# Kernel tuning notes

Hardware: AMD Instinct MI355X
Metric: run time of the kernel (lower is better)

## Reference

```python
import jax, jax.numpy as jnp
import numpy as np
from jax import lax

B, T, N, D = 64, 128, 64, 64
Q, EMB, PLM = 5, 8, 768
ALPHA = 0.5  # rarity_alpha

def _mlp(x, W1, b1, W2, b2):
    return jax.nn.relu(x @ W1 + b1) @ W2 + b2

def setup_inputs() -> dict:
    key = jax.random.key(0)
    ks = jax.random.split(key, 16)
    def xav(k, shape):
        fan_in = shape[-2] if len(shape) > 1 else shape[0]
        return jax.random.normal(k, shape, jnp.float32) / np.sqrt(fan_in)
    obs_emb = jax.random.normal(ks[0], (B, T, N, D), jnp.float32)
    observed_mask = (jax.random.uniform(ks[1], (B, T, N)) < 0.5).astype(jnp.float32)
    lengths = jax.random.randint(ks[2], (B, 1), T // 2, T + 1).astype(jnp.int32)
    lengths = lengths.at[0, 0].set(T)  # ensure max(lengths) == T like torch loop bound
    avg_interval = jax.random.uniform(ks[3], (B, T, N), jnp.float32) * 10.0
    return {
        "obs_emb": obs_emb, "observed_mask": observed_mask,
        "lengths": lengths, "avg_interval": avg_interval,
        "var_plm_rep": jax.random.normal(ks[4], (N, PLM), jnp.float32),
        "rarity_W": jax.random.normal(ks[5], (N, N), jnp.float32),
        "Wf1": xav(ks[6], (PLM, 2 * D)), "bf1": jnp.zeros((2 * D,), jnp.float32),
        "Wf2": xav(ks[7], (2 * D, Q)), "bf2": jnp.zeros((Q,), jnp.float32),
        "Wg1": xav(ks[8], (PLM, 2 * D)), "bg1": jnp.zeros((2 * D,), jnp.float32),
        "Wg2": xav(ks[9], (2 * D, EMB)), "bg2": jnp.zeros((EMB,), jnp.float32),
        "Wu": xav(ks[10], (Q, 2 * D + 1, D)), "bu": xav(ks[11], (Q, D)),
        "Wr": xav(ks[12], (Q, 2 * D + 1, D)), "br": xav(ks[13], (Q, D)),
        "Wc": xav(ks[14], (Q, 2 * D + 1, D)), "bc": xav(ks[15], (Q, D)),
    }

def reference(obs_emb, observed_mask, lengths, avg_interval, var_plm_rep, rarity_W,
              Wf1, bf1, Wf2, bf2, Wg1, bg1, Wg2, bg2, Wu, bu, Wr, br, Wc, bc):
    Bb, Tt, Nn, Dd = obs_emb.shape
    m_all = observed_mask.astype(obs_emb.dtype)                 # [B,T,N]
    # plm reps are repeated across batch in torch -> batch-identical, keep [N,*]
    qv = _mlp(var_plm_rep, Wf1, bf1, Wf2, bf2)                  # [N,Q]
    ne = _mlp(var_plm_rep, Wg1, bg1, Wg2, bg2)                  # [N,EMB]
    ne = ne / jnp.linalg.norm(ne, axis=-1, keepdims=True)
    adj = jax.nn.softmax(ne @ ne.T, axis=-1)                    # [N,N]
    # time-invariant per-node hypernetwork weights (MLP_Param einsums hoisted)
    Wr_n = jnp.einsum('nq,qio->nio', qv, Wr); br_n = qv @ br    # [N,2D+1,D],[N,D]
    Wu_n = jnp.einsum('nq,qio->nio', qv, Wu); bu_n = qv @ bu
    Wc_n = jnp.einsum('nq,qio->nio', qv, Wc); bc_n = qv @ bc
    I = jnp.eye(Nn, dtype=obs_emb.dtype)
    var_total = m_all.sum(axis=1)                               # [B,N]
    lens = lengths[:, 0]

    def step(carry, inp):
        h, out = carry
        x_t, m_t, ai_t, t = inp                                 # [B,N,D],[B,N],[B,N],[]
        rs = ALPHA * jnp.tanh(ai_t / (var_total + 1.0))         # rarity score [B,N]
        x = jnp.concatenate([x_t, rs[..., None]], axis=-1)      # [B,N,D+1]
        combined = jnp.concatenate([x, h], axis=-1)             # [B,N,2D+1]
        R = -rarity_W[None] * jnp.abs(rs[:, :, None] - rs[:, None, :])
        am = m_t[:, :, None] * m_t[:, None, :]                  # masked adjacency support
        A = adj[None] * (1.0 + R) * am * (1.0 - I) + I          # [B,N,N]
        msg = jnp.einsum('bij,bjf->bif', A, combined)           # dense message passing
        r = jax.nn.sigmoid(jnp.einsum('bnf,nfo->bno', msg, Wr_n) + br_n)
        u = jax.nn.sigmoid(jnp.einsum('bnf,nfo->bno', msg, Wu_n) + bu_n)
        upd = m_t[..., None] > 0                                # observed-node scatter mask
        h_r = jnp.where(upd, r * h, h)
        comb2 = jnp.concatenate([x, h_r], axis=-1)              # NOTE: no adj matmul here (as in torch)
        cand = jnp.tanh(jnp.einsum('bnf,nfo->bno', comb2, Wc_n) + bc_n)
        h_new = jnp.where(upd, (1.0 - u) * h_r + u * cand, h)
        out_new = jnp.where((t == lens - 1)[:, None, None], h_new, out)
        return (h_new, out_new), None

    h0 = jnp.zeros((Bb, Nn, Dd), obs_emb.dtype)
    xs = (obs_emb.swapaxes(0, 1), m_all.swapaxes(0, 1),
          avg_interval.swapaxes(0, 1), jnp.arange(Tt))
    (_, out), _ = lax.scan(step, (h0, jnp.zeros_like(h0)), xs)
    return out
```

## Files before the change

### kernel.cpp

```cpp
#include <hip/hip_runtime.h>
#include <cstddef>
#include <cstdint>

#define B_ 64
#define T_ 128
#define N_ 64
#define D_ 64
#define Q_ 5
#define E_ 8
#define P_ 768
#define H_ 128

typedef _Float16 f16;
typedef _Float16 f16x2 __attribute__((ext_vector_type(2)));
typedef _Float16 f16x4 __attribute__((ext_vector_type(4)));
typedef _Float16 f16x8 __attribute__((ext_vector_type(8)));
typedef float f32x4 __attribute__((ext_vector_type(4)));

__global__ void k_mlps(const float* __restrict__ vpr,
                       const float* __restrict__ Wf1, const float* __restrict__ bf1,
                       const float* __restrict__ Wf2, const float* __restrict__ bf2,
                       const float* __restrict__ Wg1, const float* __restrict__ bg1,
                       const float* __restrict__ Wg2, const float* __restrict__ bg2,
                       float* __restrict__ qv, float* __restrict__ neb) {
  int n = blockIdx.x;
  int tid = threadIdx.x;
  __shared__ float v[P_];
  __shared__ float hid[H_];
  __shared__ float tmp[E_];

  for (int i = tid; i < P_; i += 256) v[i] = vpr[n * P_ + i];
  __syncthreads();

  for (int j = tid; j < H_; j += 256) {
    float a = bf1[j];
#pragma unroll 8
    for (int i = 0; i < P_; ++i) a += v[i] * Wf1[i * H_ + j];
    hid[j] = fmaxf(a, 0.f);
  }
  __syncthreads();
  if (tid < Q_) {
    float a = bf2[tid];
    for (int j = 0; j < H_; ++j) a += hid[j] * Wf2[j * Q_ + tid];
    qv[n * Q_ + tid] = a;
  }
  __syncthreads();

  for (int j = tid; j < H_; j += 256) {
    float a = bg1[j];
#pragma unroll 8
    for (int i = 0; i < P_; ++i) a += v[i] * Wg1[i * H_ + j];
    hid[j] = fmaxf(a, 0.f);
  }
  __syncthreads();
  if (tid < E_) {
    float a = bg2[tid];
    for (int j = 0; j < H_; ++j) a += hid[j] * Wg2[j * E_ + tid];
    tmp[tid] = a;
  }
  __syncthreads();
  if (tid == 0) {
    float s = 0.f;
    for (int e = 0; e < E_; ++e) s += tmp[e] * tmp[e];
    float r = 1.f / sqrtf(s);
    for (int e = 0; e < E_; ++e) neb[n * E_ + e] = tmp[e] * r;
  }
}

__global__ void k_meta(const float* __restrict__ neb, const float* __restrict__ qv,
                       const float* __restrict__ br, const float* __restrict__ bu,
                       const float* __restrict__ bc,
                       const float* __restrict__ Wr, const float* __restrict__ Wu,
                       const float* __restrict__ Wc,
                       float* __restrict__ adj, float* __restrict__ brn,
                       float* __restrict__ bun, float* __restrict__ bcn,
                       float* __restrict__ WrsR, float* __restrict__ WrsU,
                       float* __restrict__ WrsC) {
  int n = blockIdx.x;
  int j = threadIdx.x;
  float s = 0.f;
#pragma unroll
  for (int e = 0; e < E_; ++e) s += neb[n * E_ + e] * neb[j * E_ + e];
  float m = s;
  for (int off = 32; off; off >>= 1) m = fmaxf(m, __shfl_xor(m, off));
  float ex = expf(s - m);
  float sum = ex;
  for (int off = 32; off; off >>= 1) sum += __shfl_xor(sum, off);
  adj[n * N_ + j] = ex / sum;

  float pr = 0.f, pu = 0.f, pc = 0.f;
  float wr = 0.f, wu = 0.f, wc = 0.f;
#pragma unroll
  for (int q = 0; q < Q_; ++q) {
    float qq = qv[n * Q_ + q];
    pr += qq * br[q * D_ + j];
    pu += qq * bu[q * D_ + j];
    pc += qq * bc[q * D_ + j];
    wr += qq * Wr[((size_t)q * 129 + 64) * D_ + j];
    wu += qq * Wu[((size_t)q * 129 + 64) * D_ + j];
    wc += qq * Wc[((size_t)q * 129 + 64) * D_ + j];
  }
  brn[n * D_ + j] = pr;
  bun[n * D_ + j] = pu;
  bcn[n * D_ + j] = pc;
  WrsR[n * D_ + j] = wr;
  WrsU[n * D_ + j] = wu;
  WrsC[n * D_ + j] = wc;
}

__global__ void k_pack(const float* __restrict__ Wr, const float* __restrict__ Wu,
                       const float* __restrict__ Wc, f16* __restrict__ Wpk) {
  int bid = blockIdx.x;
  int nt = bid & 3;
  int kt = (bid >> 2) & 3;
  int q = (bid >> 4) % 5;
  int g = bid / 80;
  const float* W = (g == 0) ? Wr : ((g == 1) ? Wu : Wc);
  int l = threadIdx.x;
  int co = 16 * nt + (l & 15);
  f16* dst = Wpk + (size_t)bid * 512 + l * 8;
#pragma unroll
  for (int e = 0; e < 8; ++e) {
    int k = 32 * kt + 8 * (l >> 4) + e;
    int f = k + (k >= 64);
    dst[e] = (f16)W[((size_t)q * 129 + f) * D_ + co];
  }
}

__global__ void k_vt(const float* __restrict__ mask, float* __restrict__ vt) {
  int b = blockIdx.x;
  int n = threadIdx.x;
  float s = 0.f;
  for (int t = 0; t < T_; ++t) s += mask[(b * T_ + t) * N_ + n];
  vt[b * N_ + n] = s;
}

__launch_bounds__(1024, 1)
__global__ void k_seq(const float* __restrict__ obs, const float* __restrict__ mask,
                      const int* __restrict__ lengths, const float* __restrict__ ai,
                      const float* __restrict__ adjG, const float* __restrict__ rarw,
                      const float* __restrict__ brn, const float* __restrict__ bun,
                      const float* __restrict__ bcn, const float* __restrict__ WrsR,
                      const float* __restrict__ WrsU, const float* __restrict__ WrsC,
                      const float* __restrict__ qv, const float* __restrict__ vt,
                      const f16* __restrict__ Wpk, float* __restrict__ out) {
  __shared__ __align__(16) f16 combT[128 * 72];
  __shared__ __align__(16) f16 AmatPre2[64 * 72];
  __shared__ __align__(16) f16 actA[64 * 136];
  __shared__ __align__(16) f16 xA[64 * 72];
  __shared__ __align__(16) f16 pre1[64 * 68];
  __shared__ __align__(16) f16 qvS[64 * 8];
  __shared__ float rsS[64];
  __shared__ float mS[64];
  __shared__ float vtS[64];
  __shared__ float mrS[64];

  const int tid = threadIdx.x;
  const int b = blockIdx.x;
  const int lane = tid & 63;
  const int wv = tid >> 6;
  const int lm = lane & 15;
  const int lq = lane >> 4;

  const int en = tid >> 4;
  const int eo = (tid & 15) * 4;

  float h[4] = {0.f, 0.f, 0.f, 0.f};

  f16x2 bRp[2], bUp[2], bCp[2], wRp[2], wUp[2], wCp[2];
  {
    float4 v;
    v = *(const float4*)(brn + en * D_ + eo);
    bRp[0] = f16x2{(f16)v.x, (f16)v.y}; bRp[1] = f16x2{(f16)v.z, (f16)v.w};
    v = *(const float4*)(bun + en * D_ + eo);
    bUp[0] = f16x2{(f16)v.x, (f16)v.y}; bUp[1] = f16x2{(f16)v.z, (f16)v.w};
    v = *(const float4*)(bcn + en * D_ + eo);
    bCp[0] = f16x2{(f16)v.x, (f16)v.y}; bCp[1] = f16x2{(f16)v.z, (f16)v.w};
    v = *(const float4*)(WrsR + en * D_ + eo);
    wRp[0] = f16x2{(f16)v.x, (f16)v.y}; wRp[1] = f16x2{(f16)v.z, (f16)v.w};
    v = *(const float4*)(WrsU + en * D_ + eo);
    wUp[0] = f16x2{(f16)v.x, (f16)v.y}; wUp[1] = f16x2{(f16)v.z, (f16)v.w};
    v = *(const float4*)(WrsC + en * D_ + eo);
    wCp[0] = f16x2{(f16)v.x, (f16)v.y}; wCp[1] = f16x2{(f16)v.z, (f16)v.w};
  }

  if (tid < 512) {
    int n = tid >> 3, q = tid & 7;
    qvS[n * 8 + q] = (q < Q_) ? (f16)qv[n * Q_ + q] : (f16)0.f;
  }
  if (tid < 64) vtS[tid] = vt[b * N_ + tid];
  for (int i = tid; i < 64 * 72; i += 1024) combT[64 * 72 + i] = (f16)0.f;
  const int lenm1 = lengths[b] - 1;
  __syncthreads();

  for (int t = 0; t < T_; ++t) {
    if (tid < 64) {
      float mv = mask[(b * T_ + t) * N_ + tid];
      float av = ai[(b * T_ + t) * N_ + tid];
      mS[tid] = mv;
      rsS[tid] = 0.5f * tanhf(av / (vtS[tid] + 1.f));
    }
    {
      float4 xv = *(const float4*)(obs + (size_t)(b * T_ + t) * (N_ * D_) + en * D_ + eo);
      f16x4 xh = {(f16)xv.x, (f16)xv.y, (f16)xv.z, (f16)xv.w};
      *(f16x4*)(xA + en * 72 + eo) = xh;
      combT[(eo + 0) * 72 + en] = xh[0];
      combT[(eo + 1) * 72 + en] = xh[1];
      combT[(eo + 2) * 72 + en] = xh[2];
      combT[(eo + 3) * 72 + en] = xh[3];
    }
    __syncthreads();

    {
      const int i = en, j0 = eo;
      float4 ad = *(const float4*)(adjG + i * N_ + j0);
      float4 rw = *(const float4*)(rarw + i * N_ + j0);
      float ri = rsS[i], mi = mS[i];
      float a0 = ad.x * (1.f - rw.x * fabsf(ri - rsS[j0 + 0])) * mi * mS[j0 + 0];
      float a1 = ad.y * (1.f - rw.y * fabsf(ri - rsS[j0 + 1])) * mi * mS[j0 + 1];
      float a2 = ad.z * (1.f - rw.z * fabsf(ri - rsS[j0 + 2])) * mi * mS[j0 + 2];
      float a3 = ad.w * (1.f - rw.w * fabsf(ri - rsS[j0 + 3])) * mi * mS[j0 + 3];
      if (i == j0 + 0) a0 = 1.f;
      if (i == j0 + 1) a1 = 1.f;
      if (i == j0 + 2) a2 = 1.f;
      if (i == j0 + 3) a3 = 1.f;
      f16x4 av = {(f16)a0, (f16)a1, (f16)a2, (f16)a3};
      *(f16x4*)(AmatPre2 + i * 72 + j0) = av;
    }
    __syncthreads();

    {
#pragma unroll
      for (int s = 0; s < 2; ++s) {
        int tt = wv * 2 + s;
        int mt = tt >> 3, ft = tt & 7;
        f32x4 acc = {0.f, 0.f, 0.f, 0.f};
#pragma unroll
        for (int kt = 0; kt < 2; ++kt) {
          int j0 = 8 * lq + 32 * kt;
          f16x8 aF = *(const f16x8*)(AmatPre2 + (lm + 16 * mt) * 72 + j0);
          f16x8 bF = *(const f16x8*)(combT + (lm + 16 * ft) * 72 + j0);
          acc = __builtin_amdgcn_mfma_f32_16x16x32_f16(aF, bF, acc, 0, 0, 0);
        }
        int row = 16 * mt + 4 * lq;
        int col = 16 * ft + lm;
        actA[(row + 0) * 136 + col] = (f16)acc[0];
        actA[(row + 1) * 136 + col] = (f16)acc[1];
        actA[(row + 2) * 136 + col] = (f16)acc[2];
        actA[(row + 3) * 136 + col] = (f16)acc[3];
      }
      if (wv == 15) {
        float s = 0.f;
        for (int j = 0; j < 64; j += 2) {
          f16x2 a2 = *(const f16x2*)(AmatPre2 + lane * 72 + j);
          s += (float)a2[0] * rsS[j] + (float)a2[1] * rsS[j + 1];
        }
        mrS[lane] = s;
      }
    }
    __syncthreads();

    f32x4 cacc[4];
    if (wv < 8) {
      const int g = wv >> 2;
      const int nt = wv & 3;
      f32x4 acc[4] = {{0.f, 0.f, 0.f, 0.f}, {0.f, 0.f, 0.f, 0.f},
                      {0.f, 0.f, 0.f, 0.f}, {0.f, 0.f, 0.f, 0.f}};
      f16x8 qh[4];
#pragma unroll
      for (int mt = 0; mt < 4; ++mt)
        qh[mt] = *(const f16x8*)(qvS + (lm + 16 * mt) * 8);
#pragma unroll
      for (int kt = 0; kt < 4; ++kt) {
        f16x8 aF[4];
#pragma unroll
        for (int mt = 0; mt < 4; ++mt)
          aF[mt] = *(const f16x8*)(actA + (lm + 16 * mt) * 136 + 8 * lq + 32 * kt);
#pragma unroll
        for (int q = 0; q < 5; ++q) {
          f16x8 wF = *(const f16x8*)(Wpk +
              ((size_t)(((g * 5 + q) * 4 + kt) * 4 + nt) * 64 + lane) * 8);
#pragma unroll
          for (int mt = 0; mt < 4; ++mt) {
            f16x8 as = aF[mt] * qh[mt][q];
            acc[mt] = __builtin_amdgcn_mfma_f32_16x16x32_f16(as, wF, acc[mt], 0, 0, 0);
          }
        }
      }
      f16* dst = g ? AmatPre2 : pre1;
#pragma unroll
      for (int mt = 0; mt < 4; ++mt) {
        int row = 16 * mt + 4 * lq;
        int col = 16 * nt + lm;
        dst[(row + 0) * 68 + col] = (f16)acc[mt][0];
        dst[(row + 1) * 68 + col] = (f16)acc[mt][1];
        dst[(row + 2) * 68 + col] = (f16)acc[mt][2];
        dst[(row + 3) * 68 + col] = (f16)acc[mt][3];
      }
    } else if (wv < 12) {
      const int nt = wv - 8;
#pragma unroll
      for (int mt = 0; mt < 4; ++mt) cacc[mt] = f32x4{0.f, 0.f, 0.f, 0.f};
      f16x8 qh[4];
#pragma unroll
      for (int mt = 0; mt < 4; ++mt)
        qh[mt] = *(const f16x8*)(qvS + (lm + 16 * mt) * 8);
#pragma unroll
      for (int kt = 0; kt < 2; ++kt) {
        f16x8 aF[4];
#pragma unroll
        for (int mt = 0; mt < 4; ++mt)
          aF[mt] = *(const f16x8*)(xA + (lm + 16 * mt) * 72 + 8 * lq + 32 * kt);
#pragma unroll
        for (int q = 0; q < 5; ++q) {
          f16x8 wF = *(const f16x8*)(Wpk +
              ((size_t)(((2 * 5 + q) * 4 + kt) * 4 + nt) * 64 + lane) * 8);
#pragma unroll
          for (int mt = 0; mt < 4; ++mt) {
            f16x8 as = aF[mt] * qh[mt][q];
            cacc[mt] = __builtin_amdgcn_mfma_f32_16x16x32_f16(as, wF, cacc[mt], 0, 0, 0);
          }
        }
      }
    }
    __syncthreads();

    float uq[4], hrq[4];
    const bool upd = mS[en] > 0.f;
    {
      f16x4 pR = *(const f16x4*)(pre1 + en * 68 + eo);
      f16x4 pU = *(const f16x4*)(AmatPre2 + en * 68 + eo);
      float mr = mrS[en];
      f16x4 hrh;
#pragma unroll
      for (int k = 0; k < 4; ++k) {
        float preR = (float)pR[k] + mr * (float)wRp[k >> 1][k & 1] + (float)bRp[k >> 1][k & 1];
        float preU = (float)pU[k] + mr * (float)wUp[k >> 1][k & 1] + (float)bUp[k >> 1][k & 1];
        float r = 1.f / (1.f + expf(-preR));
        float u = 1.f / (1.f + expf(-preU));
        float hr = upd ? r * h[k] : h[k];
        uq[k] = u;
        hrq[k] = hr;
        hrh[k] = (f16)hr;
      }
      *(f16x4*)(actA + en * 136 + 64 + eo) = hrh;
    }
    __syncthreads();

    if (wv >= 8 && wv < 12) {
      const int nt = wv - 8;
      f16x8 qh[4];
#pragma unroll
      for (int mt = 0; mt < 4; ++mt)
        qh[mt] = *(const f16x8*)(qvS + (lm + 16 * mt) * 8);
#pragma unroll
      for (int kt = 2; kt < 4; ++kt) {
        f16x8 aF[4];
#pragma unroll
        for (int mt = 0; mt < 4; ++mt)
          aF[mt] = *(const f16x8*)(actA + (lm + 16 * mt) * 136 + 8 * lq + 32 * kt);
#pragma unroll
        for (int q = 0; q < 5; ++q) {
          f16x8 wF = *(const f16x8*)(Wpk +
              ((size_t)(((2 * 5 + q) * 4 + kt) * 4 + nt) * 64 + lane) * 8);
#pragma unroll
          for (int mt = 0; mt < 4; ++mt) {
            f16x8 as = aF[mt] * qh[mt][q];
            cacc[mt] = __builtin_amdgcn_mfma_f32_16x16x32_f16(as, wF, cacc[mt], 0, 0, 0);
          }
        }
      }
#pragma unroll
      for (int mt = 0; mt < 4; ++mt) {
        int row = 16 * mt + 4 * lq;
        int col = 16 * nt + lm;
        pre1[(row + 0) * 68 + col] = (f16)cacc[mt][0];
        pre1[(row + 1) * 68 + col] = (f16)cacc[mt][1];
        pre1[(row + 2) * 68 + col] = (f16)cacc[mt][2];
        pre1[(row + 3) * 68 + col] = (f16)cacc[mt][3];
      }
    }
    __syncthreads();

    {
      f16x4 pC = *(const f16x4*)(pre1 + en * 68 + eo);
      float rsv = rsS[en];
#pragma unroll
      for (int k = 0; k < 4; ++k) {
        float pc = (float)pC[k] + rsv * (float)wCp[k >> 1][k & 1] + (float)bCp[k >> 1][k & 1];
        float cand = tanhf(pc);
        float hn = upd ? (1.f - uq[k]) * hrq[k] + uq[k] * cand : h[k];
        h[k] = hn;
        combT[(64 + eo + k) * 72 + en] = (f16)hn;
      }
      if (t == lenm1) {
        float4 o4 = {h[0], h[1], h[2], h[3]};
        *(float4*)(out + ((size_t)b * N_ + en) * D_ + eo) = o4;
      }
    }
    __syncthreads();
  }
}

extern "C" void kernel_launch(void* const* d_in, const int* in_sizes, int n_in,
                              void* d_out, int out_size, void* d_ws, size_t ws_size,
                              hipStream_t stream) {
  const float* obs  = (const float*)d_in[0];
  const float* mask = (const float*)d_in[1];
  const int*   lens = (const int*)d_in[2];
  const float* ai   = (const float*)d_in[3];
  const float* vpr  = (const float*)d_in[4];
  const float* rarw = (const float*)d_in[5];
  const float* Wf1 = (const float*)d_in[6],  *bf1 = (const float*)d_in[7];
  const float* Wf2 = (const float*)d_in[8],  *bf2 = (const float*)d_in[9];
  const float* Wg1 = (const float*)d_in[10], *bg1 = (const float*)d_in[11];
  const float* Wg2 = (const float*)d_in[12], *bg2 = (const float*)d_in[13];
  const float* Wu = (const float*)d_in[14], *bu = (const float*)d_in[15];
  const float* Wr = (const float*)d_in[16], *br = (const float*)d_in[17];
  const float* Wc = (const float*)d_in[18], *bc = (const float*)d_in[19];

  char* p = (char*)d_ws;
  auto carve = [&](size_t bytes) {
    char* r = p;
    p += (bytes + 255) & ~(size_t)255;
    return r;
  };
  float* qv   = (float*)carve(N_ * Q_ * 4);
  float* neb  = (float*)carve(N_ * E_ * 4);
  float* adj  = (float*)carve(N_ * N_ * 4);
  float* brn  = (float*)carve(N_ * D_ * 4);
  float* bun  = (float*)carve(N_ * D_ * 4);
  float* bcn  = (float*)carve(N_ * D_ * 4);
  float* WrsR = (float*)carve(N_ * D_ * 4);
  float* WrsU = (float*)carve(N_ * D_ * 4);
  float* WrsC = (float*)carve(N_ * D_ * 4);
  float* vt   = (float*)carve(B_ * N_ * 4);
  f16* Wpk    = (f16*)carve((size_t)3 * 5 * 4 * 4 * 64 * 8 * 2);

  k_mlps<<<N_, 256, 0, stream>>>(vpr, Wf1, bf1, Wf2, bf2, Wg1, bg1, Wg2, bg2, qv, neb);
  k_meta<<<N_, 64, 0, stream>>>(neb, qv, br, bu, bc, Wr, Wu, Wc,
                                adj, brn, bun, bcn, WrsR, WrsU, WrsC);
  k_pack<<<240, 64, 0, stream>>>(Wr, Wu, Wc, Wpk);
  k_vt<<<B_, 64, 0, stream>>>(mask, vt);
  k_seq<<<B_, 1024, 0, stream>>>(obs, mask, lens, ai, adj, rarw,
                                 brn, bun, bcn, WrsR, WrsU, WrsC,
                                 qv, vt, Wpk, (float*)d_out);
}
```

Measured before the change: 2.153 ms.

## Restructure recurrent kernel to 512 threads with register-resident weights and prefetch

```diff
diff --git a/kernel.cpp b/kernel.cpp
--- a/kernel.cpp
+++ b/kernel.cpp
@@ -16,6 +16,13 @@
 typedef _Float16 f16x4 __attribute__((ext_vector_type(4)));
 typedef _Float16 f16x8 __attribute__((ext_vector_type(8)));
 typedef float f32x4 __attribute__((ext_vector_type(4)));
+
+__device__ __forceinline__ float fast_sig(float x) {
+  return 1.f / (1.f + __expf(-x));
+}
+__device__ __forceinline__ float fast_tanh(float x) {
+  return 1.f - 2.f / (1.f + __expf(2.f * x));
+}
 
 __global__ void k_mlps(const float* __restrict__ vpr,
                        const float* __restrict__ Wf1, const float* __restrict__ bf1,
@@ -26,37 +33,36 @@
   int n = blockIdx.x;
   int tid = threadIdx.x;
   __shared__ float v[P_];
-  __shared__ float hid[H_];
+  __shared__ float hf[H_];
+  __shared__ float hg[H_];
   __shared__ float tmp[E_];
 
   for (int i = tid; i < P_; i += 256) v[i] = vpr[n * P_ + i];
   __syncthreads();
 
-  for (int j = tid; j < H_; j += 256) {
+  if (tid < H_) {
+    int j = tid;
     float a = bf1[j];
 #pragma unroll 8
     for (int i = 0; i < P_; ++i) a += v[i] * Wf1[i * H_ + j];
-    hid[j] = fmaxf(a, 0.f);
+    hf[j] = fmaxf(a, 0.f);
+  } else {
+    int j = tid - H_;
+    float a = bg1[j];
+#pragma unroll 8
+    for (int i = 0; i < P_; ++i) a += v[i] * Wg1[i * H_ + j];
+    hg[j] = fmaxf(a, 0.f);
   }
   __syncthreads();
   if (tid < Q_) {
     float a = bf2[tid];
-    for (int j = 0; j < H_; ++j) a += hid[j] * Wf2[j * Q_ + tid];
+    for (int j = 0; j < H_; ++j) a += hf[j] * Wf2[j * Q_ + tid];
     qv[n * Q_ + tid] = a;
-  }
-  __syncthreads();
-
-  for (int j = tid; j < H_; j += 256) {
-    float a = bg1[j];
-#pragma unroll 8
-    for (int i = 0; i < P_; ++i) a += v[i] * Wg1[i * H_ + j];
-    hid[j] = fmaxf(a, 0.f);
-  }
-  __syncthreads();
-  if (tid < E_) {
-    float a = bg2[tid];
-    for (int j = 0; j < H_; ++j) a += hid[j] * Wg2[j * E_ + tid];
-    tmp[tid] = a;
+  } else if (tid >= 8 && tid < 8 + E_) {
+    int e = tid - 8;
+    float a = bg2[e];
+    for (int j = 0; j < H_; ++j) a += hg[j] * Wg2[j * E_ + e];
+    tmp[e] = a;
   }
   __syncthreads();
   if (tid == 0) {
@@ -71,8 +77,8 @@
                        const float* __restrict__ br, const float* __restrict__ bu,
                        const float* __restrict__ bc,
                        const float* __restrict__ Wr, const float* __restrict__ Wu,
-                       const float* __restrict__ Wc,
-                       float* __restrict__ adj, float* __restrict__ brn,
+                       const float* __restrict__ Wc, const float* __restrict__ rarw,
+                       f16x2* __restrict__ adjP, float* __restrict__ brn,
                        float* __restrict__ bun, float* __restrict__ bcn,
                        float* __restrict__ WrsR, float* __restrict__ WrsU,
                        float* __restrict__ WrsC) {
@@ -83,10 +89,11 @@
   for (int e = 0; e < E_; ++e) s += neb[n * E_ + e] * neb[j * E_ + e];
   float m = s;
   for (int off = 32; off; off >>= 1) m = fmaxf(m, __shfl_xor(m, off));
-  float ex = expf(s - m);
+  float ex = __expf(s - m);
   float sum = ex;
   for (int off = 32; off; off >>= 1) sum += __shfl_xor(sum, off);
-  adj[n * N_ + j] = ex / sum;
+  float av = ex / sum;
+  adjP[n * N_ + j] = f16x2{(f16)av, (f16)(av * rarw[n * N_ + j])};
 
   float pr = 0.f, pu = 0.f, pc = 0.f;
   float wr = 0.f, wu = 0.f, wc = 0.f;
@@ -135,25 +142,24 @@
   vt[b * N_ + n] = s;
 }
 
-__launch_bounds__(1024, 1)
+__launch_bounds__(512, 1)
 __global__ void k_seq(const float* __restrict__ obs, const float* __restrict__ mask,
                       const int* __restrict__ lengths, const float* __restrict__ ai,
-                      const float* __restrict__ adjG, const float* __restrict__ rarw,
+                      const f16x2* __restrict__ adjP,
                       const float* __restrict__ brn, const float* __restrict__ bun,
                       const float* __restrict__ bcn, const float* __restrict__ WrsR,
                       const float* __restrict__ WrsU, const float* __restrict__ WrsC,
                       const float* __restrict__ qv, const float* __restrict__ vt,
                       const f16* __restrict__ Wpk, float* __restrict__ out) {
   __shared__ __align__(16) f16 combT[128 * 72];
-  __shared__ __align__(16) f16 AmatPre2[64 * 72];
   __shared__ __align__(16) f16 actA[64 * 136];
   __shared__ __align__(16) f16 xA[64 * 72];
-  __shared__ __align__(16) f16 pre1[64 * 68];
+  __shared__ __align__(16) f16 AP[64 * 72];
+  __shared__ __align__(16) f16 pCH[64 * 68];
   __shared__ __align__(16) f16 qvS[64 * 8];
-  __shared__ float rsS[64];
-  __shared__ float mS[64];
-  __shared__ float vtS[64];
-  __shared__ float mrS[64];
+  __shared__ float rsS[N_];
+  __shared__ float mS[N_];
+  __shared__ float mrS[N_];
 
   const int tid = threadIdx.x;
   const int b = blockIdx.x;
@@ -161,85 +167,134 @@
   const int wv = tid >> 6;
   const int lm = lane & 15;
   const int lq = lane >> 4;
-
-  const int en = tid >> 4;
-  const int eo = (tid & 15) * 4;
-
-  float h[4] = {0.f, 0.f, 0.f, 0.f};
-
-  f16x2 bRp[2], bUp[2], bCp[2], wRp[2], wUp[2], wCp[2];
+  const bool isU = (wv < 4);
+  const int nt = wv & 3;
+  const int oc = 16 * nt + lm;
+
+  f16x8 wA[4][5];
+  f16x8 wB[2][5];
   {
-    float4 v;
-    v = *(const float4*)(brn + en * D_ + eo);
-    bRp[0] = f16x2{(f16)v.x, (f16)v.y}; bRp[1] = f16x2{(f16)v.z, (f16)v.w};
-    v = *(const float4*)(bun + en * D_ + eo);
-    bUp[0] = f16x2{(f16)v.x, (f16)v.y}; bUp[1] = f16x2{(f16)v.z, (f16)v.w};
-    v = *(const float4*)(bcn + en * D_ + eo);
-    bCp[0] = f16x2{(f16)v.x, (f16)v.y}; bCp[1] = f16x2{(f16)v.z, (f16)v.w};
-    v = *(const float4*)(WrsR + en * D_ + eo);
-    wRp[0] = f16x2{(f16)v.x, (f16)v.y}; wRp[1] = f16x2{(f16)v.z, (f16)v.w};
-    v = *(const float4*)(WrsU + en * D_ + eo);
-    wUp[0] = f16x2{(f16)v.x, (f16)v.y}; wUp[1] = f16x2{(f16)v.z, (f16)v.w};
-    v = *(const float4*)(WrsC + en * D_ + eo);
-    wCp[0] = f16x2{(f16)v.x, (f16)v.y}; wCp[1] = f16x2{(f16)v.z, (f16)v.w};
-  }
-
-  if (tid < 512) {
-    int n = tid >> 3, q = tid & 7;
-    qvS[n * 8 + q] = (q < Q_) ? (f16)qv[n * Q_ + q] : (f16)0.f;
-  }
-  if (tid < 64) vtS[tid] = vt[b * N_ + tid];
-  for (int i = tid; i < 64 * 72; i += 1024) combT[64 * 72 + i] = (f16)0.f;
+    const int gA = isU ? 1 : 0;
+    const int ktB0 = isU ? 0 : 2;
+#pragma unroll
+    for (int kt = 0; kt < 4; ++kt)
+#pragma unroll
+      for (int q = 0; q < 5; ++q)
+        wA[kt][q] = *(const f16x8*)(Wpk +
+            ((size_t)(((gA * 5 + q) * 4 + kt) * 4 + nt) * 64 + lane) * 8);
+#pragma unroll
+    for (int kk = 0; kk < 2; ++kk)
+#pragma unroll
+      for (int q = 0; q < 5; ++q)
+        wB[kk][q] = *(const f16x8*)(Wpk +
+            ((size_t)(((2 * 5 + q) * 4 + (ktB0 + kk)) * 4 + nt) * 64 + lane) * 8);
+  }
+
+  f16x2 b1[8], b2[8], b3[8], b4[8];
+  {
+    const float* p1 = isU ? bun : brn;
+    const float* p2 = isU ? WrsU : WrsR;
+#pragma unroll
+    for (int mt = 0; mt < 4; ++mt)
+#pragma unroll
+      for (int ii = 0; ii < 2; ++ii) {
+        int n0 = 16 * mt + 4 * lq + 2 * ii;
+        b1[mt * 2 + ii] = f16x2{(f16)p1[n0 * D_ + oc], (f16)p1[(n0 + 1) * D_ + oc]};
+        b2[mt * 2 + ii] = f16x2{(f16)p2[n0 * D_ + oc], (f16)p2[(n0 + 1) * D_ + oc]};
+        if (!isU) {
+          b3[mt * 2 + ii] = f16x2{(f16)bcn[n0 * D_ + oc], (f16)bcn[(n0 + 1) * D_ + oc]};
+          b4[mt * 2 + ii] = f16x2{(f16)WrsC[n0 * D_ + oc], (f16)WrsC[(n0 + 1) * D_ + oc]};
+        } else {
+          b3[mt * 2 + ii] = f16x2{(f16)0.f, (f16)0.f};
+          b4[mt * 2 + ii] = f16x2{(f16)0.f, (f16)0.f};
+        }
+      }
+  }
+
+  f16x2 adjR[8];
+  {
+    const f16x2* arow = adjP + (tid >> 3) * N_ + 8 * (tid & 7);
+#pragma unroll
+    for (int k = 0; k < 8; ++k) adjR[k] = arow[k];
+  }
+
+  qvS[tid] = ((tid & 7) < Q_) ? (f16)qv[(tid >> 3) * Q_ + (tid & 7)] : (f16)0.f;
+  for (int i = tid; i < 64 * 72; i += 512) combT[64 * 72 + i] = (f16)0.f;
+
+  f32x4 h[4];
+#pragma unroll
+  for (int mt = 0; mt < 4; ++mt) h[mt] = f32x4{0.f, 0.f, 0.f, 0.f};
+
+  const float* xbase = obs + (size_t)b * T_ * (N_ * D_);
+  float4 xc0 = *(const float4*)(xbase + tid * 8);
+  float4 xc1 = *(const float4*)(xbase + tid * 8 + 4);
+  float mCur = 0.f, aCur = 0.f, vtR = 0.f;
+  if (tid < N_) {
+    vtR = vt[b * N_ + tid];
+    mCur = mask[(b * T_) * N_ + tid];
+    aCur = ai[(b * T_) * N_ + tid];
+  }
   const int lenm1 = lengths[b] - 1;
   __syncthreads();
 
   for (int t = 0; t < T_; ++t) {
-    if (tid < 64) {
-      float mv = mask[(b * T_ + t) * N_ + tid];
-      float av = ai[(b * T_ + t) * N_ + tid];
-      mS[tid] = mv;
-      rsS[tid] = 0.5f * tanhf(av / (vtS[tid] + 1.f));
+    if (tid < N_) {
+      mS[tid] = mCur;
+      rsS[tid] = 0.5f * fast_tanh(aCur / (vtR + 1.f));
     }
     {
-      float4 xv = *(const float4*)(obs + (size_t)(b * T_ + t) * (N_ * D_) + en * D_ + eo);
-      f16x4 xh = {(f16)xv.x, (f16)xv.y, (f16)xv.z, (f16)xv.w};
-      *(f16x4*)(xA + en * 72 + eo) = xh;
-      combT[(eo + 0) * 72 + en] = xh[0];
-      combT[(eo + 1) * 72 + en] = xh[1];
-      combT[(eo + 2) * 72 + en] = xh[2];
-      combT[(eo + 3) * 72 + en] = xh[3];
+      int n = tid >> 3, d0 = 8 * (tid & 7);
+      f16x8 xh = {(f16)xc0.x, (f16)xc0.y, (f16)xc0.z, (f16)xc0.w,
+                  (f16)xc1.x, (f16)xc1.y, (f16)xc1.z, (f16)xc1.w};
+      *(f16x8*)(xA + n * 72 + d0) = xh;
+    }
+    if (t + 1 < T_) {
+      const float* xn = xbase + (size_t)(t + 1) * (N_ * D_) + tid * 8;
+      xc0 = *(const float4*)xn;
+      xc1 = *(const float4*)(xn + 4);
+      if (tid < N_) {
+        mCur = mask[(b * T_ + t + 1) * N_ + tid];
+        aCur = ai[(b * T_ + t + 1) * N_ + tid];
+      }
     }
     __syncthreads();
 
     {
-      const int i = en, j0 = eo;
-      float4 ad = *(const float4*)(adjG + i * N_ + j0);
-      float4 rw = *(const float4*)(rarw + i * N_ + j0);
+      int i = tid >> 3, j0 = 8 * (tid & 7);
       float ri = rsS[i], mi = mS[i];
-      float a0 = ad.x * (1.f - rw.x * fabsf(ri - rsS[j0 + 0])) * mi * mS[j0 + 0];
-      float a1 = ad.y * (1.f - rw.y * fabsf(ri - rsS[j0 + 1])) * mi * mS[j0 + 1];
-      float a2 = ad.z * (1.f - rw.z * fabsf(ri - rsS[j0 + 2])) * mi * mS[j0 + 2];
-      float a3 = ad.w * (1.f - rw.w * fabsf(ri - rsS[j0 + 3])) * mi * mS[j0 + 3];
-      if (i == j0 + 0) a0 = 1.f;
-      if (i == j0 + 1) a1 = 1.f;
-      if (i == j0 + 2) a2 = 1.f;
-      if (i == j0 + 3) a3 = 1.f;
-      f16x4 av = {(f16)a0, (f16)a1, (f16)a2, (f16)a3};
-      *(f16x4*)(AmatPre2 + i * 72 + j0) = av;
+      float4 rj0 = *(const float4*)&rsS[j0];
+      float4 rj1 = *(const float4*)&rsS[j0 + 4];
+      float4 mj0 = *(const float4*)&mS[j0];
+      float4 mj1 = *(const float4*)&mS[j0 + 4];
+      float rj[8] = {rj0.x, rj0.y, rj0.z, rj0.w, rj1.x, rj1.y, rj1.z, rj1.w};
+      float mj[8] = {mj0.x, mj0.y, mj0.z, mj0.w, mj1.x, mj1.y, mj1.z, mj1.w};
+      f16x8 av;
+#pragma unroll
+      for (int k = 0; k < 8; ++k) {
+        float a = ((float)adjR[k][0] - (float)adjR[k][1] * fabsf(ri - rj[k])) * mi * mj[k];
+        if (i == j0 + k) a = 1.f;
+        av[k] = (f16)a;
+      }
+      *(f16x8*)(AP + i * 72 + j0) = av;
+
+      int d = tid >> 3, n0 = 8 * (tid & 7);
+      f16x8 tx;
+#pragma unroll
+      for (int k = 0; k < 8; ++k) tx[k] = xA[(n0 + k) * 72 + d];
+      *(f16x8*)(combT + d * 72 + n0) = tx;
     }
     __syncthreads();
 
     {
 #pragma unroll
-      for (int s = 0; s < 2; ++s) {
-        int tt = wv * 2 + s;
+      for (int s = 0; s < 4; ++s) {
+        int tt = wv * 4 + s;
         int mt = tt >> 3, ft = tt & 7;
         f32x4 acc = {0.f, 0.f, 0.f, 0.f};
 #pragma unroll
         for (int kt = 0; kt < 2; ++kt) {
-          int j0 = 8 * lq + 32 * kt;
-          f16x8 aF = *(const f16x8*)(AmatPre2 + (lm + 16 * mt) * 72 + j0);
-          f16x8 bF = *(const f16x8*)(combT + (lm + 16 * ft) * 72 + j0);
+          f16x8 aF = *(const f16x8*)(AP + (lm + 16 * mt) * 72 + 8 * lq + 32 * kt);
+          f16x8 bF = *(const f16x8*)(combT + (lm + 16 * ft) * 72 + 8 * lq + 32 * kt);
           acc = __builtin_amdgcn_mfma_f32_16x16x32_f16(aF, bF, acc, 0, 0, 0);
         }
         int row = 16 * mt + 4 * lq;
@@ -249,23 +304,24 @@
         actA[(row + 2) * 136 + col] = (f16)acc[2];
         actA[(row + 3) * 136 + col] = (f16)acc[3];
       }
-      if (wv == 15) {
-        float s = 0.f;
-        for (int j = 0; j < 64; j += 2) {
-          f16x2 a2 = *(const f16x2*)(AmatPre2 + lane * 72 + j);
-          s += (float)a2[0] * rsS[j] + (float)a2[1] * rsS[j + 1];
-        }
-        mrS[lane] = s;
-      }
-    }
-    __syncthreads();
-
-    f32x4 cacc[4];
-    if (wv < 8) {
-      const int g = wv >> 2;
-      const int nt = wv & 3;
-      f32x4 acc[4] = {{0.f, 0.f, 0.f, 0.f}, {0.f, 0.f, 0.f, 0.f},
-                      {0.f, 0.f, 0.f, 0.f}, {0.f, 0.f, 0.f, 0.f}};
+      int n = tid >> 3, j0 = 8 * (tid & 7);
+      f16x8 a8 = *(const f16x8*)(AP + n * 72 + j0);
+      float4 r0 = *(const float4*)&rsS[j0];
+      float4 r1 = *(const float4*)&rsS[j0 + 4];
+      float s = (float)a8[0] * r0.x + (float)a8[1] * r0.y + (float)a8[2] * r0.z +
+                (float)a8[3] * r0.w + (float)a8[4] * r1.x + (float)a8[5] * r1.y +
+                (float)a8[6] * r1.z + (float)a8[7] * r1.w;
+      s += __shfl_xor(s, 1);
+      s += __shfl_xor(s, 2);
+      s += __shfl_xor(s, 4);
+      if ((lane & 7) == 0) mrS[n] = s;
+    }
+    __syncthreads();
+
+    f32x4 gacc[4];
+#pragma unroll
+    for (int mt = 0; mt < 4; ++mt) gacc[mt] = f32x4{0.f, 0.f, 0.f, 0.f};
+    {
       f16x8 qh[4];
 #pragma unroll
       for (int mt = 0; mt < 4; ++mt)
@@ -278,124 +334,131 @@
           aF[mt] = *(const f16x8*)(actA + (lm + 16 * mt) * 136 + 8 * lq + 32 * kt);
 #pragma unroll
         for (int q = 0; q < 5; ++q) {
-          f16x8 wF = *(const f16x8*)(Wpk +
-              ((size_t)(((g * 5 + q) * 4 + kt) * 4 + nt) * 64 + lane) * 8);
+          f16x8 wF = wA[kt][q];
 #pragma unroll
           for (int mt = 0; mt < 4; ++mt) {
             f16x8 as = aF[mt] * qh[mt][q];
-            acc[mt] = __builtin_amdgcn_mfma_f32_16x16x32_f16(as, wF, acc[mt], 0, 0, 0);
+            gacc[mt] = __builtin_amdgcn_mfma_f32_16x16x32_f16(as, wF, gacc[mt], 0, 0, 0);
           }
         }
       }
-      f16* dst = g ? AmatPre2 : pre1;
+    }
+    if (!isU) {
 #pragma unroll
       for (int mt = 0; mt < 4; ++mt) {
-        int row = 16 * mt + 4 * lq;
-        int col = 16 * nt + lm;
-        dst[(row + 0) * 68 + col] = (f16)acc[mt][0];
-        dst[(row + 1) * 68 + col] = (f16)acc[mt][1];
-        dst[(row + 2) * 68 + col] = (f16)acc[mt][2];
-        dst[(row + 3) * 68 + col] = (f16)acc[mt][3];
-      }
-    } else if (wv < 12) {
-      const int nt = wv - 8;
-#pragma unroll
-      for (int mt = 0; mt < 4; ++mt) cacc[mt] = f32x4{0.f, 0.f, 0.f, 0.f};
+        float4 mr4 = *(const float4*)&mrS[16 * mt + 4 * lq];
+#pragma unroll
+        for (int i = 0; i < 4; ++i) {
+          float bb = (float)b1[mt * 2 + (i >> 1)][i & 1];
+          float ww = (float)b2[mt * 2 + (i >> 1)][i & 1];
+          float v = gacc[mt][i] + bb + mr4[i] * ww;
+          AP[(16 * mt + 4 * lq + i) * 68 + oc] = (f16)fast_sig(v);
+        }
+      }
+    }
+    __syncthreads();
+
+    f16x2 upk[8];
+    if (isU) {
+#pragma unroll
+      for (int mt = 0; mt < 4; ++mt) {
+        float4 mr4 = *(const float4*)&mrS[16 * mt + 4 * lq];
+        float4 m4 = *(const float4*)&mS[16 * mt + 4 * lq];
+#pragma unroll
+        for (int i = 0; i < 4; ++i) {
+          int row = 16 * mt + 4 * lq + i;
+          float bb = (float)b1[mt * 2 + (i >> 1)][i & 1];
+          float ww = (float)b2[mt * 2 + (i >> 1)][i & 1];
+          float u = fast_sig(gacc[mt][i] + bb + mr4[i] * ww);
+          float rt = (float)AP[row * 68 + oc];
+          float hr = (m4[i] > 0.f) ? rt * h[mt][i] : h[mt][i];
+          upk[mt * 2 + (i >> 1)][i & 1] = (f16)u;
+          actA[row * 136 + 64 + oc] = (f16)hr;
+        }
+      }
+    }
+    __syncthreads();
+
+    f32x4 cacc[4];
+#pragma unroll
+    for (int mt = 0; mt < 4; ++mt) cacc[mt] = f32x4{0.f, 0.f, 0.f, 0.f};
+    {
       f16x8 qh[4];
 #pragma unroll
       for (int mt = 0; mt < 4; ++mt)
         qh[mt] = *(const f16x8*)(qvS + (lm + 16 * mt) * 8);
-#pragma unroll
-      for (int kt = 0; kt < 2; ++kt) {
-        f16x8 aF[4];
-#pragma unroll
-        for (int mt = 0; mt < 4; ++mt)
-          aF[mt] = *(const f16x8*)(xA + (lm + 16 * mt) * 72 + 8 * lq + 32 * kt);
-#pragma unroll
-        for (int q = 0; q < 5; ++q) {
-          f16x8 wF = *(const f16x8*)(Wpk +
-              ((size_t)(((2 * 5 + q) * 4 + kt) * 4 + nt) * 64 + lane) * 8);
-#pragma unroll
-          for (int mt = 0; mt < 4; ++mt) {
-            f16x8 as = aF[mt] * qh[mt][q];
-            cacc[mt] = __builtin_amdgcn_mfma_f32_16x16x32_f16(as, wF, cacc[mt], 0, 0, 0);
+      if (isU) {
+#pragma unroll
+        for (int kk = 0; kk < 2; ++kk) {
+          f16x8 aF[4];
+#pragma unroll
+          for (int mt = 0; mt < 4; ++mt)
+            aF[mt] = *(const f16x8*)(xA + (lm + 16 * mt) * 72 + 8 * lq + 32 * kk);
+#pragma unroll
+          for (int q = 0; q < 5; ++q) {
+            f16x8 wF = wB[kk][q];
+#pragma unroll
+            for (int mt = 0; mt < 4; ++mt) {
+              f16x8 as = aF[mt] * qh[mt][q];
+              cacc[mt] = __builtin_amdgcn_mfma_f32_16x16x32_f16(as, wF, cacc[mt], 0, 0, 0);
+            }
           }
         }
-      }
-    }
-    __syncthreads();
-
-    float uq[4], hrq[4];
-    const bool upd = mS[en] > 0.f;
-    {
-      f16x4 pR = *(const f16x4*)(pre1 + en * 68 + eo);
-      f16x4 pU = *(const f16x4*)(AmatPre2 + en * 68 + eo);
-      float mr = mrS[en];
-      f16x4 hrh;
-#pragma unroll
-      for (int k = 0; k < 4; ++k) {
-        float preR = (float)pR[k] + mr * (float)wRp[k >> 1][k & 1] + (float)bRp[k >> 1][k & 1];
-        float preU = (float)pU[k] + mr * (float)wUp[k >> 1][k & 1] + (float)bUp[k >> 1][k & 1];
-        float r = 1.f / (1.f + expf(-preR));
-        float u = 1.f / (1.f + expf(-preU));
-        float hr = upd ? r * h[k] : h[k];
-        uq[k] = u;
-        hrq[k] = hr;
-        hrh[k] = (f16)hr;
-      }
-      *(f16x4*)(actA + en * 136 + 64 + eo) = hrh;
-    }
-    __syncthreads();
-
-    if (wv >= 8 && wv < 12) {
-      const int nt = wv - 8;
-      f16x8 qh[4];
-#pragma unroll
-      for (int mt = 0; mt < 4; ++mt)
-        qh[mt] = *(const f16x8*)(qvS + (lm + 16 * mt) * 8);
-#pragma unroll
-      for (int kt = 2; kt < 4; ++kt) {
-        f16x8 aF[4];
-#pragma unroll
-        for (int mt = 0; mt < 4; ++mt)
-          aF[mt] = *(const f16x8*)(actA + (lm + 16 * mt) * 136 + 8 * lq + 32 * kt);
-#pragma unroll
-        for (int q = 0; q < 5; ++q) {
-          f16x8 wF = *(const f16x8*)(Wpk +
-              ((size_t)(((2 * 5 + q) * 4 + kt) * 4 + nt) * 64 + lane) * 8);
-#pragma unroll
-          for (int mt = 0; mt < 4; ++mt) {
-            f16x8 as = aF[mt] * qh[mt][q];
-            cacc[mt] = __builtin_amdgcn_mfma_f32_16x16x32_f16(as, wF, cacc[mt], 0, 0, 0);
+      } else {
+#pragma unroll
+        for (int kk = 0; kk < 2; ++kk) {
+          int kt = 2 + kk;
+          f16x8 aF[4];
+#pragma unroll
+          for (int mt = 0; mt < 4; ++mt)
+            aF[mt] = *(const f16x8*)(actA + (lm + 16 * mt) * 136 + 8 * lq + 32 * kt);
+#pragma unroll
+          for (int q = 0; q < 5; ++q) {
+            f16x8 wF = wB[kk][q];
+#pragma unroll
+            for (int mt = 0; mt < 4; ++mt) {
+              f16x8 as = aF[mt] * qh[mt][q];
+              cacc[mt] = __builtin_amdgcn_mfma_f32_16x16x32_f16(as, wF, cacc[mt], 0, 0, 0);
+            }
           }
         }
-      }
+#pragma unroll
+        for (int mt = 0; mt < 4; ++mt) {
+          float4 rs4 = *(const float4*)&rsS[16 * mt + 4 * lq];
+#pragma unroll
+          for (int i = 0; i < 4; ++i) {
+            float bb = (float)b3[mt * 2 + (i >> 1)][i & 1];
+            float ww = (float)b4[mt * 2 + (i >> 1)][i & 1];
+            float v = cacc[mt][i] + bb + rs4[i] * ww;
+            pCH[(16 * mt + 4 * lq + i) * 68 + oc] = (f16)v;
+          }
+        }
+      }
+    }
+    __syncthreads();
+
+    if (isU) {
 #pragma unroll
       for (int mt = 0; mt < 4; ++mt) {
-        int row = 16 * mt + 4 * lq;
-        int col = 16 * nt + lm;
-        pre1[(row + 0) * 68 + col] = (f16)cacc[mt][0];
-        pre1[(row + 1) * 68 + col] = (f16)cacc[mt][1];
-        pre1[(row + 2) * 68 + col] = (f16)cacc[mt][2];
-        pre1[(row + 3) * 68 + col] = (f16)cacc[mt][3];
-      }
-    }
-    __syncthreads();
-
-    {
-      f16x4 pC = *(const f16x4*)(pre1 + en * 68 + eo);
-      float rsv = rsS[en];
-#pragma unroll
-      for (int k = 0; k < 4; ++k) {
-        float pc = (float)pC[k] + rsv * (float)wCp[k >> 1][k & 1] + (float)bCp[k >> 1][k & 1];
-        float cand = tanhf(pc);
-        float hn = upd ? (1.f - uq[k]) * hrq[k] + uq[k] * cand : h[k];
-        h[k] = hn;
-        combT[(64 + eo + k) * 72 + en] = (f16)hn;
-      }
-      if (t == lenm1) {
-        float4 o4 = {h[0], h[1], h[2], h[3]};
-        *(float4*)(out + ((size_t)b * N_ + en) * D_ + eo) = o4;
+        float4 m4 = *(const float4*)&mS[16 * mt + 4 * lq];
+        f16x4 hquad;
+#pragma unroll
+        for (int i = 0; i < 4; ++i) {
+          int row = 16 * mt + 4 * lq + i;
+          float pc = cacc[mt][i] + (float)pCH[row * 68 + oc];
+          float cand = fast_tanh(pc);
+          float u = (float)upk[mt * 2 + (i >> 1)][i & 1];
+          float hr = (float)actA[row * 136 + 64 + oc];
+          float hn = (m4[i] > 0.f) ? (1.f - u) * hr + u * cand : h[mt][i];
+          h[mt][i] = hn;
+          hquad[i] = (f16)hn;
+        }
+        *(f16x4*)(combT + (64 + oc) * 72 + 16 * mt + 4 * lq) = hquad;
+        if (t == lenm1) {
+#pragma unroll
+          for (int i = 0; i < 4; ++i)
+            out[((size_t)b * N_ + 16 * mt + 4 * lq + i) * D_ + oc] = h[mt][i];
+        }
       }
     }
     __syncthreads();
@@ -427,7 +490,7 @@
   };
   float* qv   = (float*)carve(N_ * Q_ * 4);
   float* neb  = (float*)carve(N_ * E_ * 4);
-  float* adj  = (float*)carve(N_ * N_ * 4);
+  f16x2* adjP = (f16x2*)carve(N_ * N_ * 4);
   float* brn  = (float*)carve(N_ * D_ * 4);
   float* bun  = (float*)carve(N_ * D_ * 4);
   float* bcn  = (float*)carve(N_ * D_ * 4);
@@ -438,11 +501,11 @@
   f16* Wpk    = (f16*)carve((size_t)3 * 5 * 4 * 4 * 64 * 8 * 2);
 
   k_mlps<<<N_, 256, 0, stream>>>(vpr, Wf1, bf1, Wf2, bf2, Wg1, bg1, Wg2, bg2, qv, neb);
-  k_meta<<<N_, 64, 0, stream>>>(neb, qv, br, bu, bc, Wr, Wu, Wc,
-                                adj, brn, bun, bcn, WrsR, WrsU, WrsC);
+  k_meta<<<N_, 64, 0, stream>>>(neb, qv, br, bu, bc, Wr, Wu, Wc, rarw,
+                                adjP, brn, bun, bcn, WrsR, WrsU, WrsC);
   k_pack<<<240, 64, 0, stream>>>(Wr, Wu, Wc, Wpk);
   k_vt<<<B_, 64, 0, stream>>>(mask, vt);
-  k_seq<<<B_, 1024, 0, stream>>>(obs, mask, lens, ai, adj, rarw,
-                                 brn, bun, bcn, WrsR, WrsU, WrsC,
-                                 qv, vt, Wpk, (float*)d_out);
-}
+  k_seq<<<B_, 512, 0, stream>>>(obs, mask, lens, ai, adjP,
+                                brn, bun, bcn, WrsR, WrsU, WrsC,
+                                qv, vt, Wpk, (float*)d_out);
+}
```

New measurement: 2.552 ms. +18.5%, slower.
